# Performance work log

Measured on AMD Instinct MI355X. Metric: run time of the kernel, lower is better.

The kernel has to match this reference:

```python
import jax, jax.numpy as jnp
import numpy as np

N_USER = 50000
N_ITEM = 50000
E = 800000
C_IN = 128
C_OUT = 128
N_HEADS = 4


def setup_inputs() -> dict:
    key = jax.random.key(0)
    ks = jax.random.split(key, 12)
    xav = lambda k, shp: jax.random.uniform(k, shp, jnp.float32, -1.0, 1.0) * jnp.sqrt(6.0 / (shp[0] + shp[1]))
    return {
        'x_user': jax.random.normal(ks[0], (N_USER, C_IN), jnp.float32),
        'x_item': jax.random.normal(ks[1], (N_ITEM, C_IN), jnp.float32),
        'ei_u2i': jnp.stack([jax.random.randint(ks[2], (E,), 0, N_USER, jnp.int32),
                             jax.random.randint(ks[3], (E,), 0, N_ITEM, jnp.int32)]),
        'ei_i2u': jnp.stack([jax.random.randint(ks[4], (E,), 0, N_ITEM, jnp.int32),
                             jax.random.randint(ks[5], (E,), 0, N_USER, jnp.int32)]),
        'W_nb': xav(ks[6], (C_OUT, C_IN)),
        'b_nb': jnp.zeros((C_OUT,), jnp.float32),
        'W_self': xav(ks[7], (C_OUT, C_IN)),
        'b_self': jnp.zeros((C_OUT,), jnp.float32),
        'in_proj_w': xav(ks[8], (3 * C_OUT, C_OUT)),
        'in_proj_b': jnp.zeros((3 * C_OUT,), jnp.float32),
        'out_proj_w': xav(ks[9], (C_OUT, C_OUT)),
        'out_proj_b': jnp.zeros((C_OUT,), jnp.float32),
    }


def _multi_aggr(h_src, edge_index, n_dst):
    """h_src: already lin_neighbor-transformed src features [N_src, C].
    Returns [n_dst, 4, C] stacked as [max, min, sum, mean] (torch_scatter semantics:
    empty segments -> 0; mean divides by clamp(count, 1))."""
    src, dst = edge_index[0], edge_index[1]
    msgs = h_src[src]  # [E, C]  (linear commutes with gather)
    s = jax.ops.segment_sum(msgs, dst, num_segments=n_dst)
    cnt = jax.ops.segment_sum(jnp.ones((msgs.shape[0],), msgs.dtype), dst, num_segments=n_dst)
    has = (cnt > 0)[:, None]
    mean = s / jnp.maximum(cnt, 1.0)[:, None]
    mx = jnp.where(has, jax.ops.segment_max(msgs, dst, num_segments=n_dst), 0.0)
    mn = jnp.where(has, jax.ops.segment_min(msgs, dst, num_segments=n_dst), 0.0)
    return jnp.stack([mx, mn, s, mean], axis=1)  # [n_dst, 4, C]


def _mha(tokens, in_proj_w, in_proj_b, out_proj_w, out_proj_b):
    """torch nn.MultiheadAttention (eval mode, batch_first=False). tokens: [S, N, C]."""
    S, N, C = tokens.shape
    H, Dh = N_HEADS, C // N_HEADS
    qkv = tokens @ in_proj_w.T + in_proj_b            # [S, N, 3C]
    q, k, v = jnp.split(qkv, 3, axis=-1)
    q = q.reshape(S, N, H, Dh) * (1.0 / jnp.sqrt(jnp.asarray(Dh, tokens.dtype)))
    k = k.reshape(S, N, H, Dh)
    v = v.reshape(S, N, H, Dh)
    scores = jnp.einsum('snhd,tnhd->nhst', q, k)       # [N, H, S, S]
    attn = jax.nn.softmax(scores, axis=-1)
    o = jnp.einsum('nhst,tnhd->snhd', attn, v).reshape(S, N, C)
    return o @ out_proj_w.T + out_proj_b               # [S, N, C]


def reference(x_user, x_item, ei_u2i, ei_i2u, W_nb, b_nb, W_self, b_self,
              in_proj_w, in_proj_b, out_proj_w, out_proj_b):
    # shared neighbor linear applied once per node type, then gathered per edge
    h_user = x_user @ W_nb.T + b_nb
    h_item = x_item @ W_nb.T + b_nb
    aggr_item = _multi_aggr(h_user, ei_u2i, N_ITEM)    # user->item : [N_item, 4, C]
    aggr_user = _multi_aggr(h_item, ei_i2u, N_USER)    # item->user : [N_user, 4, C]

    def per_type(x, aggr):
        self_feat = x @ W_self.T + b_self              # [N, C]
        # tokens: [self, max, min, sum, mean] -> [5, N, C]
        tokens = jnp.concatenate([self_feat[None], jnp.transpose(aggr, (1, 0, 2))], axis=0)
        attn_out = _mha(tokens, in_proj_w, in_proj_b, out_proj_w, out_proj_b)
        return self_feat + attn_out.mean(axis=0)

    out_user = per_type(x_user, aggr_user)
    out_item = per_type(x_item, aggr_item)
    return (out_user, out_item)
```

## Files before the change

kernel.cpp:

```cpp
#include <hip/hip_runtime.h>
#include <hip/hip_bf16.h>


#define C 128
#define NHEAD 4
#define DH 32
#define QK_SCALE 0.17677669529663687f

typedef __attribute__((ext_vector_type(8))) short bf16x8;
typedef __attribute__((ext_vector_type(4))) short short4v;
typedef __attribute__((ext_vector_type(2))) short short2v;
typedef __attribute__((ext_vector_type(4))) float f32x4;

__device__ __forceinline__ short f2bf(float f) {
    unsigned u = __float_as_uint(f);
    unsigned r = u + 0x7FFFu + ((u >> 16) & 1u);
    return (short)(r >> 16);
}

__global__ __launch_bounds__(256, 2) void transform_kernel(
    const float* __restrict__ xu, const float* __restrict__ xi,
    int NU, int NTOT,
    const float* __restrict__ Wnb, const float* __restrict__ bnb,
    const float* __restrict__ Wself, const float* __restrict__ bself,
    float* __restrict__ h, float* __restrict__ selfout)
{
    __shared__ float As[64 * 132];
    __shared__ float Bs[256 * 36];
    __shared__ float biasS[256];

    const int tid = threadIdx.x;
    const int row0 = blockIdx.x * 64;

    biasS[tid] = (tid < 128) ? bnb[tid] : bself[tid - 128];

#pragma unroll
    for (int i = 0; i < 8; i++) {
        int id = tid + i * 256;
        int r = id >> 5, c4 = id & 31;
        int row = row0 + r;
        float4 v = make_float4(0.f, 0.f, 0.f, 0.f);
        if (row < NTOT) {
            v = (row < NU) ? ((const float4*)xu)[(size_t)row * 32 + c4]
                           : ((const float4*)xi)[(size_t)(row - NU) * 32 + c4];
        }
        *(float4*)&As[r * 132 + c4 * 4] = v;
    }

    const int tm = tid >> 5;
    const int tn = tid & 31;

    float acc[8][8];
#pragma unroll
    for (int m = 0; m < 8; m++)
#pragma unroll
        for (int j = 0; j < 8; j++) acc[m][j] = 0.f;

    for (int ks = 0; ks < 4; ks++) {
        __syncthreads();
#pragma unroll
        for (int i = 0; i < 8; i++) {
            int id = tid + i * 256;
            int n = id >> 3, q = id & 7;
            const float4* src = (n < 128)
                ? &((const float4*)Wnb)[(size_t)n * 32 + ks * 8 + q]
                : &((const float4*)Wself)[(size_t)(n - 128) * 32 + ks * 8 + q];
            *(float4*)&Bs[n * 36 + q * 4] = *src;
        }
        __syncthreads();

        for (int k4 = 0; k4 < 8; k4++) {
            float4 a[8];
#pragma unroll
            for (int m = 0; m < 8; m++)
                a[m] = *(const float4*)&As[(tm * 8 + m) * 132 + ks * 32 + k4 * 4];
            float4 b[8];
#pragma unroll
            for (int j = 0; j < 8; j++)
                b[j] = *(const float4*)&Bs[(tn + 32 * j) * 36 + k4 * 4];
#pragma unroll
            for (int m = 0; m < 8; m++) {
                float4 av = a[m];
#pragma unroll
                for (int j = 0; j < 8; j++) {
                    float4 bv = b[j];
                    acc[m][j] += av.x * bv.x + av.y * bv.y
                               + av.z * bv.z + av.w * bv.w;
                }
            }
        }
    }

#pragma unroll
    for (int m = 0; m < 8; m++) {
        int row = row0 + tm * 8 + m;
        if (row < NTOT) {
#pragma unroll
            for (int j = 0; j < 8; j++) {
                int jj = tn + 32 * j;
                float v = acc[m][j] + biasS[jj];
                if (j < 4) h[(size_t)row * C + jj] = v;
                else       selfout[(size_t)row * C + (jj - 128)] = v;
            }
        }
    }
}

__global__ __launch_bounds__(256) void prep_kernel(
    const float* __restrict__ Wip, unsigned* __restrict__ img,
    int* __restrict__ curA, int nA, int* __restrict__ curB, int nB)
{
    const int tid = threadIdx.x;
    if (blockIdx.x < 96) {
        int id = blockIdx.x * 256 + tid;
        int ks = id / (384 * 16);
        int rem = id - ks * (384 * 16);
        int n = rem >> 4, kk = rem & 15;
        float a = Wip[(size_t)n * C + ks * 32 + kk * 2 + 0];
        float b = Wip[(size_t)n * C + ks * 32 + kk * 2 + 1];
        unsigned pa = ((unsigned)(unsigned short)f2bf(a))
                    | (((unsigned)(unsigned short)f2bf(b)) << 16);
        img[(size_t)ks * 6144 + n * 16 + kk] = pa;
    } else {
        int i = (blockIdx.x - 96) * 256 + tid;
        if (i < nA) curA[i] = 0;
        else if (i < nA + nB) curB[i - nA] = 0;
    }
}

__global__ __launch_bounds__(256) void hist2_kernel(
    const int* __restrict__ dstA, int nA, int* __restrict__ curA,
    const int* __restrict__ dstB, int nB, int* __restrict__ curB)
{
    int i = blockIdx.x * 256 + threadIdx.x;
    if (i < nA) atomicAdd(&curA[dstA[i]], 1);
    else if (i < nA + nB) atomicAdd(&curB[dstB[i - nA]], 1);
}

__global__ __launch_bounds__(1024) void scan2_kernel(
    int* __restrict__ curA, int nA, int* __restrict__ curB, int nB)
{
    int* cur = (blockIdx.x == 0) ? curA : curB;
    const int n = (blockIdx.x == 0) ? nA : nB;

    __shared__ int wsum[16];
    __shared__ int carryS;
    const int tid = threadIdx.x, lane = tid & 63, wv = tid >> 6;
    if (tid == 0) carryS = 0;
    __syncthreads();
    for (int base = 0; base < n; base += 4096) {
        int i0 = base + tid * 4;
        int v0 = 0, v1 = 0, v2 = 0, v3 = 0;
        if (i0 + 3 < n) {
            int4 t = *(const int4*)&cur[i0];
            v0 = t.x; v1 = t.y; v2 = t.z; v3 = t.w;
        } else {
            if (i0 < n) v0 = cur[i0];
            if (i0 + 1 < n) v1 = cur[i0 + 1];
            if (i0 + 2 < n) v2 = cur[i0 + 2];
            if (i0 + 3 < n) v3 = cur[i0 + 3];
        }
        int s1 = v0 + v1, s2 = s1 + v2, s3 = s2 + v3;
        int x = s3;
#pragma unroll
        for (int d = 1; d < 64; d <<= 1) {
            int t = __shfl_up(x, d, 64);
            if (lane >= d) x += t;
        }
        if (lane == 63) wsum[wv] = x;
        int carry = carryS;
        __syncthreads();
        int wpre = 0;
#pragma unroll
        for (int w2 = 0; w2 < 16; w2++) wpre += (w2 < wv) ? wsum[w2] : 0;
        int excl = x - s3 + wpre + carry;
        if (i0 + 3 < n) {
            int4 st; st.x = excl; st.y = excl + v0; st.z = excl + s1; st.w = excl + s2;
            *(int4*)&cur[i0] = st;
        } else {
            if (i0 < n) cur[i0] = excl;
            if (i0 + 1 < n) cur[i0 + 1] = excl + v0;
            if (i0 + 2 < n) cur[i0 + 2] = excl + s1;
            if (i0 + 3 < n) cur[i0 + 3] = excl + s2;
        }
        __syncthreads();
        if (tid == 0) {
            int t = 0;
#pragma unroll
            for (int w2 = 0; w2 < 16; w2++) t += wsum[w2];
            carryS = carry + t;
        }
        __syncthreads();
    }
}

__global__ __launch_bounds__(256) void fill_kernel(
    const int* __restrict__ src, const int* __restrict__ dst, int n,
    int* __restrict__ cur, int* __restrict__ csr)
{
    int i = blockIdx.x * 256 + threadIdx.x;
    if (i < n) {
        int p = atomicAdd(&cur[dst[i]], 1);
        csr[p] = src[i];
    }
}

#define ATN 4

__global__ __launch_bounds__(256, 8) void attn_fused_kernel(
    const float* __restrict__ h_src, const int* __restrict__ csr,
    const int* __restrict__ cur, const float* __restrict__ selfF,
    const short* __restrict__ wipbf, const float* __restrict__ bip,
    float* __restrict__ omean_g, int n_nodes)
{
    __shared__ char Ash[16 * 272];
    __shared__ float cinv[ATN];

    const int tid = threadIdx.x;
    const int lane = tid & 63;
    const int wv = tid >> 6;
    const int node0 = blockIdx.x * ATN;

    if (tid < 128) {
        int r = tid >> 5, c4 = tid & 31;
        int node = node0 + r;
        float4 v = make_float4(0.f, 0.f, 0.f, 0.f);
        if (node < n_nodes) v = ((const float4*)selfF)[(size_t)node * 32 + c4];
        short4v b;
        b.x = f2bf(v.x); b.y = f2bf(v.y); b.z = f2bf(v.z); b.w = f2bf(v.w);
        *(short4v*)(Ash + (r * 4) * 272 + c4 * 8) = b;
    }

    {
        const float2* h2 = (const float2*)h_src;
        int node = node0 + wv;
        float2 vs = make_float2(0.f, 0.f);
        float2 vmx = make_float2(-3.4e38f, -3.4e38f);
        float2 vmn = make_float2(3.4e38f, 3.4e38f);
        int deg = 0;
        if (node < n_nodes) {
            int start = (node == 0) ? 0 : cur[node - 1];
            int end = cur[node];
            deg = end - start;
            int e = start;
            for (; e + 8 <= end; e += 8) {
                float2 v[8];
#pragma unroll
                for (int i = 0; i < 8; i++) {
                    int s = csr[e + i];
                    v[i] = h2[(size_t)s * 64 + lane];
                }
#pragma unroll
                for (int i = 0; i < 8; i++) {
                    vs.x += v[i].x; vs.y += v[i].y;
                    vmx.x = fmaxf(vmx.x, v[i].x); vmx.y = fmaxf(vmx.y, v[i].y);
                    vmn.x = fminf(vmn.x, v[i].x); vmn.y = fminf(vmn.y, v[i].y);
                }
            }
            if (e < end) {
                int last = end - 1;
                float2 v[8];
#pragma unroll
                for (int i = 0; i < 8; i++) {
                    int idx = e + i;
                    int s = csr[(idx <= last) ? idx : last];
                    v[i] = h2[(size_t)s * 64 + lane];
                }
#pragma unroll
                for (int i = 0; i < 8; i++) {
                    if (e + i <= last) {
                        vs.x += v[i].x; vs.y += v[i].y;
                        vmx.x = fmaxf(vmx.x, v[i].x); vmx.y = fmaxf(vmx.y, v[i].y);
                        vmn.x = fminf(vmn.x, v[i].x); vmn.y = fminf(vmn.y, v[i].y);
                    }
                }
            }
        }
        if (deg == 0) {
            vmx = make_float2(0.f, 0.f);
            vmn = make_float2(0.f, 0.f);
        }
        short2v p;
        p.x = f2bf(vmx.x); p.y = f2bf(vmx.y);
        *(short2v*)(Ash + (wv * 4 + 1) * 272 + lane * 4) = p;
        p.x = f2bf(vmn.x); p.y = f2bf(vmn.y);
        *(short2v*)(Ash + (wv * 4 + 2) * 272 + lane * 4) = p;
        p.x = f2bf(vs.x); p.y = f2bf(vs.y);
        *(short2v*)(Ash + (wv * 4 + 3) * 272 + lane * 4) = p;
        if (lane == 0) cinv[wv] = 1.f / (float)max(deg, 1);
    }
    __syncthreads();

    const int quad = lane >> 4;
    const int col16 = lane & 15;

    f32x4 acc[6];
#pragma unroll
    for (int t = 0; t < 6; t++) acc[t] = (f32x4){0.f, 0.f, 0.f, 0.f};

#pragma unroll
    for (int ks = 0; ks < 4; ks++) {
        bf16x8 af = *(const bf16x8*)(Ash + col16 * 272 + ks * 64 + quad * 16);
#pragma unroll
        for (int t = 0; t < 6; t++) {
            int nb = wv * 32 + (t & 1) * 16 + (t >> 1) * 128 + col16;
            bf16x8 bfr = *(const bf16x8*)((const char*)wipbf
                          + (size_t)ks * 24576 + (size_t)nb * 64 + quad * 16);
            acc[t] = __builtin_amdgcn_mfma_f32_16x16x32_bf16(af, bfr, acc[t], 0, 0, 0);
        }
    }

    const float ci = cinv[quad];
    const float cis = ci * QK_SCALE;

    const float bq0 = bip[wv * 32 + col16];
    const float bq1 = bip[wv * 32 + 16 + col16];
    const float bk0 = bip[128 + wv * 32 + col16];
    const float bk1 = bip[128 + wv * 32 + 16 + col16];
    const float bv0 = bip[256 + wv * 32 + col16];
    const float bv1 = bip[256 + wv * 32 + 16 + col16];
    const float bq0s = bq0 * QK_SCALE;
    const float bq1s = bq1 * QK_SCALE;

    float k0[5], k1[5];
#pragma unroll
    for (int s = 0; s < 4; s++) { k0[s] = acc[2][s] + bk0; k1[s] = acc[3][s] + bk1; }
    k0[4] = fmaf(acc[2][3], ci, bk0);
    k1[4] = fmaf(acc[3][3], ci, bk1);

    float wj[5] = {0.f, 0.f, 0.f, 0.f, 0.f};
#pragma unroll
    for (int i = 0; i < 5; i++) {
        float qi0 = (i < 4) ? fmaf(acc[0][i], QK_SCALE, bq0s)
                            : fmaf(acc[0][3], cis, bq0s);
        float qi1 = (i < 4) ? fmaf(acc[1][i], QK_SCALE, bq1s)
                            : fmaf(acc[1][3], cis, bq1s);
        float sv[5];
#pragma unroll
        for (int j = 0; j < 5; j++) sv[j] = qi0 * k0[j] + qi1 * k1[j];
#pragma unroll
        for (int j = 0; j < 5; j++) {
            sv[j] += __shfl_xor(sv[j], 1, 16);
            sv[j] += __shfl_xor(sv[j], 2, 16);
            sv[j] += __shfl_xor(sv[j], 4, 16);
            sv[j] += __shfl_xor(sv[j], 8, 16);
        }
        float m = sv[0];
#pragma unroll
        for (int j = 1; j < 5; j++) m = fmaxf(m, sv[j]);
        float e[5], l = 0.f;
#pragma unroll
        for (int j = 0; j < 5; j++) { e[j] = __expf(sv[j] - m); l += e[j]; }
        float inv = 0.2f / l;
#pragma unroll
        for (int j = 0; j < 5; j++) wj[j] = fmaf(e[j], inv, wj[j]);
    }

    float o0 = 0.f, o1 = 0.f;
#pragma unroll
    for (int j = 0; j < 5; j++) {
        float v0 = (j < 4) ? (acc[4][j] + bv0) : fmaf(acc[4][3], ci, bv0);
        float v1 = (j < 4) ? (acc[5][j] + bv1) : fmaf(acc[5][3], ci, bv1);
        o0 = fmaf(wj[j], v0, o0);
        o1 = fmaf(wj[j], v1, o1);
    }

    int node = node0 + quad;
    if (node < n_nodes) {
        omean_g[(size_t)node * C + wv * 32 + col16] = o0;
        omean_g[(size_t)node * C + wv * 32 + 16 + col16] = o1;
    }
}

__global__ __launch_bounds__(256, 3) void outproj_kernel(
    const float* __restrict__ omean_g, const float* __restrict__ Wop,
    const float* __restrict__ bop, float* __restrict__ out, int M)
{
    __shared__ float As[64 * 132];
    __shared__ float Bs[128 * 36];
    __shared__ float bopS[C];

    const int tid = threadIdx.x;
    const int m0 = blockIdx.x * 64;

    if (tid < C) bopS[tid] = bop[tid];

#pragma unroll
    for (int i = 0; i < 8; i++) {
        int id = tid + i * 256;
        int r = id >> 5, c4 = id & 31;
        float4 v = make_float4(0.f, 0.f, 0.f, 0.f);
        if (m0 + r < M) v = ((const float4*)omean_g)[(size_t)(m0 + r) * 32 + c4];
        *(float4*)&As[r * 132 + c4 * 4] = v;
    }

    const int tm = tid >> 5;
    const int tn = tid & 31;

    float acc[8][4];
#pragma unroll
    for (int m = 0; m < 8; m++)
#pragma unroll
        for (int j = 0; j < 4; j++) acc[m][j] = 0.f;

    for (int ks = 0; ks < 4; ks++) {
        __syncthreads();
#pragma unroll
        for (int i = 0; i < 4; i++) {
            int id = tid + i * 256;
            int n = id >> 3, q = id & 7;
            float4 w = ((const float4*)Wop)[(size_t)n * 32 + ks * 8 + q];
            *(float4*)&Bs[n * 36 + q * 4] = w;
        }
        __syncthreads();

        for (int k4 = 0; k4 < 8; k4++) {
            float4 a[8];
#pragma unroll
            for (int m = 0; m < 8; m++)
                a[m] = *(const float4*)&As[(tm * 8 + m) * 132 + ks * 32 + k4 * 4];
            float4 b[4];
#pragma unroll
            for (int j = 0; j < 4; j++)
                b[j] = *(const float4*)&Bs[(tn + 32 * j) * 36 + k4 * 4];
#pragma unroll
            for (int m = 0; m < 8; m++) {
                float4 av = a[m];
#pragma unroll
                for (int j = 0; j < 4; j++) {
                    float4 bv = b[j];
                    acc[m][j] += av.x * bv.x + av.y * bv.y
                               + av.z * bv.z + av.w * bv.w;
                }
            }
        }
    }

#pragma unroll
    for (int m = 0; m < 8; m++) {
        int row = m0 + tm * 8 + m;
        if (row < M) {
#pragma unroll
            for (int j = 0; j < 4; j++) {
                int col = tn + 32 * j;
                float* o = &out[(size_t)row * C + col];
                *o += acc[m][j] + bopS[col];
            }
        }
    }
}

extern "C" void kernel_launch(void* const* d_in, const int* in_sizes, int n_in,
                              void* d_out, int out_size, void* d_ws, size_t ws_size,
                              hipStream_t stream) {
    const float* x_user = (const float*)d_in[0];
    const float* x_item = (const float*)d_in[1];
    const int*   ei_u2i = (const int*)d_in[2];
    const int*   ei_i2u = (const int*)d_in[3];
    const float* W_nb   = (const float*)d_in[4];
    const float* b_nb   = (const float*)d_in[5];
    const float* W_self = (const float*)d_in[6];
    const float* b_self = (const float*)d_in[7];
    const float* Wip    = (const float*)d_in[8];
    const float* bip    = (const float*)d_in[9];
    const float* Wop    = (const float*)d_in[10];
    const float* bop    = (const float*)d_in[11];

    const int NU = in_sizes[0] / C;
    const int NI = in_sizes[1] / C;
    const int E1 = in_sizes[2] / 2;
    const int E2 = in_sizes[3] / 2;
    const int NTOT = NU + NI;

    float* out_user = (float*)d_out;
    float* out_item = out_user + (size_t)NU * C;

    float* ws = (float*)d_ws;
    short* wipbf     = (short*)ws;
    float* h_all     = ws + 24576;
    const size_t rc = (size_t)NTOT * C;
    float* omean_all = h_all + rc;
    int*   curA      = (int*)(omean_all + rc);
    const int maxN   = (NU > NI) ? NU : NI;
    int*   csr       = curA + maxN;

    float* h_user = h_all;
    float* h_item = h_all + (size_t)NU * C;
    float* om_user = omean_all;
    float* om_item = omean_all + (size_t)NU * C;
    int*   curB    = (int*)om_item;

    prep_kernel<<<96 + (NTOT + 255) / 256, 256, 0, stream>>>(
        Wip, (unsigned*)wipbf, curA, NI, curB, NU);

    transform_kernel<<<(NTOT + 63) / 64, 256, 0, stream>>>(
        x_user, x_item, NU, NTOT, W_nb, b_nb, W_self, b_self, h_all, (float*)d_out);

    hist2_kernel<<<(E1 + E2 + 255) / 256, 256, 0, stream>>>(
        ei_u2i + E1, E1, curA, ei_i2u + E2, E2, curB);

    scan2_kernel<<<2, 1024, 0, stream>>>(curA, NI, curB, NU);

    fill_kernel<<<(E2 + 255) / 256, 256, 0, stream>>>(ei_i2u, ei_i2u + E2, E2, curB, csr);
    attn_fused_kernel<<<(NU + ATN - 1) / ATN, 256, 0, stream>>>(
        h_item, csr, curB, out_user, wipbf, bip, om_user, NU);

    fill_kernel<<<(E1 + 255) / 256, 256, 0, stream>>>(ei_u2i, ei_u2i + E1, E1, curA, csr);
    attn_fused_kernel<<<(NI + ATN - 1) / ATN, 256, 0, stream>>>(
        h_user, csr, curA, out_item, wipbf, bip, om_item, NI);

    outproj_kernel<<<(NTOT + 63) / 64, 256, 0, stream>>>(
        omean_all, Wop, bop, (float*)d_out, NTOT);
}
```

Measured before the change: 696.3 us.

## Merge launches, use 16-bit CSR indices, process 8 nodes per attention block

Folds the weight-prep and counter-zeroing kernel into the transform kernel as extra blocks. It also merges both fill kernels and both attention kernels into single launches over the two edge directions. CSR source indices are stored as 16-bit values to cut index traffic, and each attention block now handles 8 nodes, with each wave aggregating two nodes and running two MFMA row tiles. The aim is fewer launches and better overlap between directions. The cost is more register pressure, lower occupancy, and reliance on node counts fitting in 16 bits: 50000 does fit, but larger graphs would break.

```diff
diff --git a/kernel.cpp b/kernel.cpp
--- a/kernel.cpp
+++ b/kernel.cpp
@@ -18,18 +18,41 @@
     return (short)(r >> 16);
 }
 
-__global__ __launch_bounds__(256, 2) void transform_kernel(
+__global__ __launch_bounds__(256, 2) void transform_prep_kernel(
     const float* __restrict__ xu, const float* __restrict__ xi,
     int NU, int NTOT,
     const float* __restrict__ Wnb, const float* __restrict__ bnb,
     const float* __restrict__ Wself, const float* __restrict__ bself,
-    float* __restrict__ h, float* __restrict__ selfout)
+    float* __restrict__ h, float* __restrict__ selfout,
+    const float* __restrict__ Wip, unsigned* __restrict__ img,
+    int* __restrict__ curA, int nA, int* __restrict__ curB, int nB, int TB)
 {
+    const int tid = threadIdx.x;
+
+    if ((int)blockIdx.x >= TB) {
+        int bid2 = (int)blockIdx.x - TB;
+        if (bid2 < 96) {
+            int id = bid2 * 256 + tid;
+            int ks = id / (384 * 16);
+            int rem = id - ks * (384 * 16);
+            int n = rem >> 4, kk = rem & 15;
+            float a = Wip[(size_t)n * C + ks * 32 + kk * 2 + 0];
+            float b = Wip[(size_t)n * C + ks * 32 + kk * 2 + 1];
+            unsigned pa = ((unsigned)(unsigned short)f2bf(a))
+                        | (((unsigned)(unsigned short)f2bf(b)) << 16);
+            img[(size_t)ks * 6144 + n * 16 + kk] = pa;
+        } else {
+            int i = (bid2 - 96) * 256 + tid;
+            if (i < nA) curA[i] = 0;
+            else if (i < nA + nB) curB[i - nA] = 0;
+        }
+        return;
+    }
+
     __shared__ float As[64 * 132];
     __shared__ float Bs[256 * 36];
     __shared__ float biasS[256];
 
-    const int tid = threadIdx.x;
     const int row0 = blockIdx.x * 64;
 
     biasS[tid] = (tid < 128) ? bnb[tid] : bself[tid - 128];
@@ -103,28 +126,6 @@
                 else       selfout[(size_t)row * C + (jj - 128)] = v;
             }
         }
-    }
-}
-
-__global__ __launch_bounds__(256) void prep_kernel(
-    const float* __restrict__ Wip, unsigned* __restrict__ img,
-    int* __restrict__ curA, int nA, int* __restrict__ curB, int nB)
-{
-    const int tid = threadIdx.x;
-    if (blockIdx.x < 96) {
-        int id = blockIdx.x * 256 + tid;
-        int ks = id / (384 * 16);
-        int rem = id - ks * (384 * 16);
-        int n = rem >> 4, kk = rem & 15;
-        float a = Wip[(size_t)n * C + ks * 32 + kk * 2 + 0];
-        float b = Wip[(size_t)n * C + ks * 32 + kk * 2 + 1];
-        unsigned pa = ((unsigned)(unsigned short)f2bf(a))
-                    | (((unsigned)(unsigned short)f2bf(b)) << 16);
-        img[(size_t)ks * 6144 + n * 16 + kk] = pa;
-    } else {
-        int i = (blockIdx.x - 96) * 256 + tid;
-        if (i < nA) curA[i] = 0;
-        else if (i < nA + nB) curB[i - nA] = 0;
     }
 }
 
@@ -194,34 +195,52 @@
     }
 }
 
-__global__ __launch_bounds__(256) void fill_kernel(
-    const int* __restrict__ src, const int* __restrict__ dst, int n,
-    int* __restrict__ cur, int* __restrict__ csr)
+__global__ __launch_bounds__(256) void fill2_kernel(
+    const int* __restrict__ srcA, const int* __restrict__ dstA, int nA,
+    int* __restrict__ curA, unsigned short* __restrict__ csrA,
+    const int* __restrict__ srcB, const int* __restrict__ dstB, int nB,
+    int* __restrict__ curB, unsigned short* __restrict__ csrB)
 {
     int i = blockIdx.x * 256 + threadIdx.x;
-    if (i < n) {
-        int p = atomicAdd(&cur[dst[i]], 1);
-        csr[p] = src[i];
-    }
-}
-
-#define ATN 4
-
-__global__ __launch_bounds__(256, 8) void attn_fused_kernel(
-    const float* __restrict__ h_src, const int* __restrict__ csr,
-    const int* __restrict__ cur, const float* __restrict__ selfF,
-    const short* __restrict__ wipbf, const float* __restrict__ bip,
-    float* __restrict__ omean_g, int n_nodes)
+    if (i < nA) {
+        int p = atomicAdd(&curA[dstA[i]], 1);
+        csrA[p] = (unsigned short)srcA[i];
+    } else if (i < nA + nB) {
+        int j = i - nA;
+        int p = atomicAdd(&curB[dstB[j]], 1);
+        csrB[p] = (unsigned short)srcB[j];
+    }
+}
+
+#define ATN 8
+
+__global__ __launch_bounds__(256, 6) void attn2_kernel(
+    const float* __restrict__ hB, const unsigned short* __restrict__ csrB,
+    const int* __restrict__ curB, const float* __restrict__ selfB,
+    float* __restrict__ omB, int nNodesB, int nbB,
+    const float* __restrict__ hA, const unsigned short* __restrict__ csrA,
+    const int* __restrict__ curA, const float* __restrict__ selfA,
+    float* __restrict__ omA, int nNodesA,
+    const short* __restrict__ wipbf, const float* __restrict__ bip)
 {
-    __shared__ char Ash[16 * 272];
+    __shared__ char Ash[32 * 272];
     __shared__ float cinv[ATN];
 
     const int tid = threadIdx.x;
     const int lane = tid & 63;
     const int wv = tid >> 6;
-    const int node0 = blockIdx.x * ATN;
-
-    if (tid < 128) {
+
+    const int bid = (int)blockIdx.x;
+    const bool dirB = bid < nbB;
+    const float* h_src = dirB ? hB : hA;
+    const unsigned short* csr = dirB ? csrB : csrA;
+    const int* cur = dirB ? curB : curA;
+    const float* selfF = dirB ? selfB : selfA;
+    float* omean_g = dirB ? omB : omA;
+    const int n_nodes = dirB ? nNodesB : nNodesA;
+    const int node0 = (dirB ? bid : bid - nbB) * ATN;
+
+    {
         int r = tid >> 5, c4 = tid & 31;
         int node = node0 + r;
         float4 v = make_float4(0.f, 0.f, 0.f, 0.f);
@@ -231,9 +250,11 @@
         *(short4v*)(Ash + (r * 4) * 272 + c4 * 8) = b;
     }
 
-    {
-        const float2* h2 = (const float2*)h_src;
-        int node = node0 + wv;
+    const float2* h2 = (const float2*)h_src;
+#pragma unroll
+    for (int half = 0; half < 2; half++) {
+        int nl = wv * 2 + half;
+        int node = node0 + nl;
         float2 vs = make_float2(0.f, 0.f);
         float2 vmx = make_float2(-3.4e38f, -3.4e38f);
         float2 vmn = make_float2(3.4e38f, 3.4e38f);
@@ -282,36 +303,37 @@
         }
         short2v p;
         p.x = f2bf(vmx.x); p.y = f2bf(vmx.y);
-        *(short2v*)(Ash + (wv * 4 + 1) * 272 + lane * 4) = p;
+        *(short2v*)(Ash + (nl * 4 + 1) * 272 + lane * 4) = p;
         p.x = f2bf(vmn.x); p.y = f2bf(vmn.y);
-        *(short2v*)(Ash + (wv * 4 + 2) * 272 + lane * 4) = p;
+        *(short2v*)(Ash + (nl * 4 + 2) * 272 + lane * 4) = p;
         p.x = f2bf(vs.x); p.y = f2bf(vs.y);
-        *(short2v*)(Ash + (wv * 4 + 3) * 272 + lane * 4) = p;
-        if (lane == 0) cinv[wv] = 1.f / (float)max(deg, 1);
+        *(short2v*)(Ash + (nl * 4 + 3) * 272 + lane * 4) = p;
+        if (lane == 0) cinv[nl] = 1.f / (float)max(deg, 1);
     }
     __syncthreads();
 
     const int quad = lane >> 4;
     const int col16 = lane & 15;
 
-    f32x4 acc[6];
-#pragma unroll
-    for (int t = 0; t < 6; t++) acc[t] = (f32x4){0.f, 0.f, 0.f, 0.f};
+    f32x4 acc[2][6];
+#pragma unroll
+    for (int m = 0; m < 2; m++)
+#pragma unroll
+        for (int t = 0; t < 6; t++) acc[m][t] = (f32x4){0.f, 0.f, 0.f, 0.f};
 
 #pragma unroll
     for (int ks = 0; ks < 4; ks++) {
-        bf16x8 af = *(const bf16x8*)(Ash + col16 * 272 + ks * 64 + quad * 16);
+        bf16x8 af0 = *(const bf16x8*)(Ash + col16 * 272 + ks * 64 + quad * 16);
+        bf16x8 af1 = *(const bf16x8*)(Ash + (16 + col16) * 272 + ks * 64 + quad * 16);
 #pragma unroll
         for (int t = 0; t < 6; t++) {
             int nb = wv * 32 + (t & 1) * 16 + (t >> 1) * 128 + col16;
             bf16x8 bfr = *(const bf16x8*)((const char*)wipbf
                           + (size_t)ks * 24576 + (size_t)nb * 64 + quad * 16);
-            acc[t] = __builtin_amdgcn_mfma_f32_16x16x32_bf16(af, bfr, acc[t], 0, 0, 0);
-        }
-    }
-
-    const float ci = cinv[quad];
-    const float cis = ci * QK_SCALE;
+            acc[0][t] = __builtin_amdgcn_mfma_f32_16x16x32_bf16(af0, bfr, acc[0][t], 0, 0, 0);
+            acc[1][t] = __builtin_amdgcn_mfma_f32_16x16x32_bf16(af1, bfr, acc[1][t], 0, 0, 0);
+        }
+    }
 
     const float bq0 = bip[wv * 32 + col16];
     const float bq1 = bip[wv * 32 + 16 + col16];
@@ -322,53 +344,62 @@
     const float bq0s = bq0 * QK_SCALE;
     const float bq1s = bq1 * QK_SCALE;
 
-    float k0[5], k1[5];
-#pragma unroll
-    for (int s = 0; s < 4; s++) { k0[s] = acc[2][s] + bk0; k1[s] = acc[3][s] + bk1; }
-    k0[4] = fmaf(acc[2][3], ci, bk0);
-    k1[4] = fmaf(acc[3][3], ci, bk1);
-
-    float wj[5] = {0.f, 0.f, 0.f, 0.f, 0.f};
-#pragma unroll
-    for (int i = 0; i < 5; i++) {
-        float qi0 = (i < 4) ? fmaf(acc[0][i], QK_SCALE, bq0s)
-                            : fmaf(acc[0][3], cis, bq0s);
-        float qi1 = (i < 4) ? fmaf(acc[1][i], QK_SCALE, bq1s)
-                            : fmaf(acc[1][3], cis, bq1s);
-        float sv[5];
-#pragma unroll
-        for (int j = 0; j < 5; j++) sv[j] = qi0 * k0[j] + qi1 * k1[j];
+#pragma unroll
+    for (int m = 0; m < 2; m++) {
+        const float ci = cinv[m * 4 + quad];
+        const float cis = ci * QK_SCALE;
+
+        float k0[5], k1[5];
+#pragma unroll
+        for (int s = 0; s < 4; s++) {
+            k0[s] = acc[m][2][s] + bk0;
+            k1[s] = acc[m][3][s] + bk1;
+        }
+        k0[4] = fmaf(acc[m][2][3], ci, bk0);
+        k1[4] = fmaf(acc[m][3][3], ci, bk1);
+
+        float wj[5] = {0.f, 0.f, 0.f, 0.f, 0.f};
+#pragma unroll
+        for (int i = 0; i < 5; i++) {
+            float qi0 = (i < 4) ? fmaf(acc[m][0][i], QK_SCALE, bq0s)
+                                : fmaf(acc[m][0][3], cis, bq0s);
+            float qi1 = (i < 4) ? fmaf(acc[m][1][i], QK_SCALE, bq1s)
+                                : fmaf(acc[m][1][3], cis, bq1s);
+            float sv[5];
+#pragma unroll
+            for (int j = 0; j < 5; j++) sv[j] = qi0 * k0[j] + qi1 * k1[j];
+#pragma unroll
+            for (int j = 0; j < 5; j++) {
+                sv[j] += __shfl_xor(sv[j], 1, 16);
+                sv[j] += __shfl_xor(sv[j], 2, 16);
+                sv[j] += __shfl_xor(sv[j], 4, 16);
+                sv[j] += __shfl_xor(sv[j], 8, 16);
+            }
+            float mx = sv[0];
+#pragma unroll
+            for (int j = 1; j < 5; j++) mx = fmaxf(mx, sv[j]);
+            float e[5], l = 0.f;
+#pragma unroll
+            for (int j = 0; j < 5; j++) { e[j] = __expf(sv[j] - mx); l += e[j]; }
+            float inv = 0.2f / l;
+#pragma unroll
+            for (int j = 0; j < 5; j++) wj[j] = fmaf(e[j], inv, wj[j]);
+        }
+
+        float o0 = 0.f, o1 = 0.f;
 #pragma unroll
         for (int j = 0; j < 5; j++) {
-            sv[j] += __shfl_xor(sv[j], 1, 16);
-            sv[j] += __shfl_xor(sv[j], 2, 16);
-            sv[j] += __shfl_xor(sv[j], 4, 16);
-            sv[j] += __shfl_xor(sv[j], 8, 16);
-        }
-        float m = sv[0];
-#pragma unroll
-        for (int j = 1; j < 5; j++) m = fmaxf(m, sv[j]);
-        float e[5], l = 0.f;
-#pragma unroll
-        for (int j = 0; j < 5; j++) { e[j] = __expf(sv[j] - m); l += e[j]; }
-        float inv = 0.2f / l;
-#pragma unroll
-        for (int j = 0; j < 5; j++) wj[j] = fmaf(e[j], inv, wj[j]);
-    }
-
-    float o0 = 0.f, o1 = 0.f;
-#pragma unroll
-    for (int j = 0; j < 5; j++) {
-        float v0 = (j < 4) ? (acc[4][j] + bv0) : fmaf(acc[4][3], ci, bv0);
-        float v1 = (j < 4) ? (acc[5][j] + bv1) : fmaf(acc[5][3], ci, bv1);
-        o0 = fmaf(wj[j], v0, o0);
-        o1 = fmaf(wj[j], v1, o1);
-    }
-
-    int node = node0 + quad;
-    if (node < n_nodes) {
-        omean_g[(size_t)node * C + wv * 32 + col16] = o0;
-        omean_g[(size_t)node * C + wv * 32 + 16 + col16] = o1;
+            float v0 = (j < 4) ? (acc[m][4][j] + bv0) : fmaf(acc[m][4][3], ci, bv0);
+            float v1 = (j < 4) ? (acc[m][5][j] + bv1) : fmaf(acc[m][5][3], ci, bv1);
+            o0 = fmaf(wj[j], v0, o0);
+            o1 = fmaf(wj[j], v1, o1);
+        }
+
+        int node = node0 + m * 4 + quad;
+        if (node < n_nodes) {
+            omean_g[(size_t)node * C + wv * 32 + col16] = o0;
+            omean_g[(size_t)node * C + wv * 32 + 16 + col16] = o1;
+        }
     }
 }
 
@@ -394,9 +425,8 @@
         *(float4*)&As[r * 132 + c4 * 4] = v;
     }
 
+    const int tn = tid & 31;
     const int tm = tid >> 5;
-    const int tn = tid & 31;
-
     float acc[8][4];
 #pragma unroll
     for (int m = 0; m < 8; m++)
@@ -481,33 +511,36 @@
     const size_t rc = (size_t)NTOT * C;
     float* omean_all = h_all + rc;
     int*   curA      = (int*)(omean_all + rc);
-    const int maxN   = (NU > NI) ? NU : NI;
-    int*   csr       = curA + maxN;
+    int*   curB      = curA + NI;
+    unsigned short* csrA16 = (unsigned short*)(curB + NU);
+    unsigned short* csrB16 = csrA16 + E1;
 
     float* h_user = h_all;
     float* h_item = h_all + (size_t)NU * C;
     float* om_user = omean_all;
     float* om_item = omean_all + (size_t)NU * C;
-    int*   curB    = (int*)om_item;
-
-    prep_kernel<<<96 + (NTOT + 255) / 256, 256, 0, stream>>>(
-        Wip, (unsigned*)wipbf, curA, NI, curB, NU);
-
-    transform_kernel<<<(NTOT + 63) / 64, 256, 0, stream>>>(
-        x_user, x_item, NU, NTOT, W_nb, b_nb, W_self, b_self, h_all, (float*)d_out);
+
+    const int TB = (NTOT + 63) / 64;
+    const int PB = 96 + (NTOT + 255) / 256;
+    transform_prep_kernel<<<TB + PB, 256, 0, stream>>>(
+        x_user, x_item, NU, NTOT, W_nb, b_nb, W_self, b_self,
+        h_all, (float*)d_out, Wip, (unsigned*)wipbf, curA, NI, curB, NU, TB);
 
     hist2_kernel<<<(E1 + E2 + 255) / 256, 256, 0, stream>>>(
         ei_u2i + E1, E1, curA, ei_i2u + E2, E2, curB);
 
     scan2_kernel<<<2, 1024, 0, stream>>>(curA, NI, curB, NU);
 
-    fill_kernel<<<(E2 + 255) / 256, 256, 0, stream>>>(ei_i2u, ei_i2u + E2, E2, curB, csr);
-    attn_fused_kernel<<<(NU + ATN - 1) / ATN, 256, 0, stream>>>(
-        h_item, csr, curB, out_user, wipbf, bip, om_user, NU);
-
-    fill_kernel<<<(E1 + 255) / 256, 256, 0, stream>>>(ei_u2i, ei_u2i + E1, E1, curA, csr);
-    attn_fused_kernel<<<(NI + ATN - 1) / ATN, 256, 0, stream>>>(
-        h_user, csr, curA, out_item, wipbf, bip, om_item, NI);
+    fill2_kernel<<<(E1 + E2 + 255) / 256, 256, 0, stream>>>(
+        ei_u2i, ei_u2i + E1, E1, curA, csrA16,
+        ei_i2u, ei_i2u + E2, E2, curB, csrB16);
+
+    const int nbB = (NU + ATN - 1) / ATN;
+    const int nbA = (NI + ATN - 1) / ATN;
+    attn2_kernel<<<nbB + nbA, 256, 0, stream>>>(
+        h_item, csrB16, curB, out_user, om_user, NU, nbB,
+        h_user, csrA16, curA, out_item, om_item, NI,
+        wipbf, bip);
 
     outproj_kernel<<<(NTOT + 63) / 64, 256, 0, stream>>>(
         omean_all, Wop, bop, (float*)d_out, NTOT);
```

Measured after the change: 788.7 us. 13.3% more time.

## Fuse prep into transform, merge CSR fills, store CSR indices as uint16

Applied to the files above, without the earlier changes.

Folds the weight bf16 packing and counter zeroing into extra blocks of the transform kernel, and builds both CSR arrays in one fill kernel, removing two launches. Each edge type now gets its own CSR buffer, and source indices are stored as 16-bit values. This halves index traffic in the gather-heavy attention kernels. The uint16 indices only work while node counts stay at or below 65535, which holds for the fixed problem sizes.

```diff
diff --git a/kernel.cpp b/kernel.cpp
--- a/kernel.cpp
+++ b/kernel.cpp
@@ -18,18 +18,41 @@
     return (short)(r >> 16);
 }
 
-__global__ __launch_bounds__(256, 2) void transform_kernel(
+__global__ __launch_bounds__(256, 2) void transform_prep_kernel(
     const float* __restrict__ xu, const float* __restrict__ xi,
     int NU, int NTOT,
     const float* __restrict__ Wnb, const float* __restrict__ bnb,
     const float* __restrict__ Wself, const float* __restrict__ bself,
-    float* __restrict__ h, float* __restrict__ selfout)
+    float* __restrict__ h, float* __restrict__ selfout,
+    const float* __restrict__ Wip, unsigned* __restrict__ img,
+    int* __restrict__ curA, int nA, int* __restrict__ curB, int nB, int TB)
 {
+    const int tid = threadIdx.x;
+
+    if ((int)blockIdx.x >= TB) {
+        int bid2 = (int)blockIdx.x - TB;
+        if (bid2 < 96) {
+            int id = bid2 * 256 + tid;
+            int ks = id / (384 * 16);
+            int rem = id - ks * (384 * 16);
+            int n = rem >> 4, kk = rem & 15;
+            float a = Wip[(size_t)n * C + ks * 32 + kk * 2 + 0];
+            float b = Wip[(size_t)n * C + ks * 32 + kk * 2 + 1];
+            unsigned pa = ((unsigned)(unsigned short)f2bf(a))
+                        | (((unsigned)(unsigned short)f2bf(b)) << 16);
+            img[(size_t)ks * 6144 + n * 16 + kk] = pa;
+        } else {
+            int i = (bid2 - 96) * 256 + tid;
+            if (i < nA) curA[i] = 0;
+            else if (i < nA + nB) curB[i - nA] = 0;
+        }
+        return;
+    }
+
     __shared__ float As[64 * 132];
     __shared__ float Bs[256 * 36];
     __shared__ float biasS[256];
 
-    const int tid = threadIdx.x;
     const int row0 = blockIdx.x * 64;
 
     biasS[tid] = (tid < 128) ? bnb[tid] : bself[tid - 128];
@@ -103,28 +126,6 @@
                 else       selfout[(size_t)row * C + (jj - 128)] = v;
             }
         }
-    }
-}
-
-__global__ __launch_bounds__(256) void prep_kernel(
-    const float* __restrict__ Wip, unsigned* __restrict__ img,
-    int* __restrict__ curA, int nA, int* __restrict__ curB, int nB)
-{
-    const int tid = threadIdx.x;
-    if (blockIdx.x < 96) {
-        int id = blockIdx.x * 256 + tid;
-        int ks = id / (384 * 16);
-        int rem = id - ks * (384 * 16);
-        int n = rem >> 4, kk = rem & 15;
-        float a = Wip[(size_t)n * C + ks * 32 + kk * 2 + 0];
-        float b = Wip[(size_t)n * C + ks * 32 + kk * 2 + 1];
-        unsigned pa = ((unsigned)(unsigned short)f2bf(a))
-                    | (((unsigned)(unsigned short)f2bf(b)) << 16);
-        img[(size_t)ks * 6144 + n * 16 + kk] = pa;
-    } else {
-        int i = (blockIdx.x - 96) * 256 + tid;
-        if (i < nA) curA[i] = 0;
-        else if (i < nA + nB) curB[i - nA] = 0;
     }
 }
 
@@ -194,21 +195,27 @@
     }
 }
 
-__global__ __launch_bounds__(256) void fill_kernel(
-    const int* __restrict__ src, const int* __restrict__ dst, int n,
-    int* __restrict__ cur, int* __restrict__ csr)
+__global__ __launch_bounds__(256) void fill2_kernel(
+    const int* __restrict__ srcA, const int* __restrict__ dstA, int nA,
+    int* __restrict__ curA, unsigned short* __restrict__ csrA,
+    const int* __restrict__ srcB, const int* __restrict__ dstB, int nB,
+    int* __restrict__ curB, unsigned short* __restrict__ csrB)
 {
     int i = blockIdx.x * 256 + threadIdx.x;
-    if (i < n) {
-        int p = atomicAdd(&cur[dst[i]], 1);
-        csr[p] = src[i];
+    if (i < nA) {
+        int p = atomicAdd(&curA[dstA[i]], 1);
+        csrA[p] = (unsigned short)srcA[i];
+    } else if (i < nA + nB) {
+        int j = i - nA;
+        int p = atomicAdd(&curB[dstB[j]], 1);
+        csrB[p] = (unsigned short)srcB[j];
     }
 }
 
 #define ATN 4
 
 __global__ __launch_bounds__(256, 8) void attn_fused_kernel(
-    const float* __restrict__ h_src, const int* __restrict__ csr,
+    const float* __restrict__ h_src, const unsigned short* __restrict__ csr,
     const int* __restrict__ cur, const float* __restrict__ selfF,
     const short* __restrict__ wipbf, const float* __restrict__ bip,
     float* __restrict__ omean_g, int n_nodes)
@@ -394,9 +401,8 @@
         *(float4*)&As[r * 132 + c4 * 4] = v;
     }
 
+    const int tn = tid & 31;
     const int tm = tid >> 5;
-    const int tn = tid & 31;
-
     float acc[8][4];
 #pragma unroll
     for (int m = 0; m < 8; m++)
@@ -481,33 +487,35 @@
     const size_t rc = (size_t)NTOT * C;
     float* omean_all = h_all + rc;
     int*   curA      = (int*)(omean_all + rc);
-    const int maxN   = (NU > NI) ? NU : NI;
-    int*   csr       = curA + maxN;
+    int*   curB      = curA + NI;
+    unsigned short* csrA16 = (unsigned short*)(curB + NU);
+    unsigned short* csrB16 = csrA16 + E1;
 
     float* h_user = h_all;
     float* h_item = h_all + (size_t)NU * C;
     float* om_user = omean_all;
     float* om_item = omean_all + (size_t)NU * C;
-    int*   curB    = (int*)om_item;
-
-    prep_kernel<<<96 + (NTOT + 255) / 256, 256, 0, stream>>>(
-        Wip, (unsigned*)wipbf, curA, NI, curB, NU);
-
-    transform_kernel<<<(NTOT + 63) / 64, 256, 0, stream>>>(
-        x_user, x_item, NU, NTOT, W_nb, b_nb, W_self, b_self, h_all, (float*)d_out);
+
+    const int TB = (NTOT + 63) / 64;
+    const int PB = 96 + (NTOT + 255) / 256;
+    transform_prep_kernel<<<TB + PB, 256, 0, stream>>>(
+        x_user, x_item, NU, NTOT, W_nb, b_nb, W_self, b_self,
+        h_all, (float*)d_out, Wip, (unsigned*)wipbf, curA, NI, curB, NU, TB);
 
     hist2_kernel<<<(E1 + E2 + 255) / 256, 256, 0, stream>>>(
         ei_u2i + E1, E1, curA, ei_i2u + E2, E2, curB);
 
     scan2_kernel<<<2, 1024, 0, stream>>>(curA, NI, curB, NU);
 
-    fill_kernel<<<(E2 + 255) / 256, 256, 0, stream>>>(ei_i2u, ei_i2u + E2, E2, curB, csr);
+    fill2_kernel<<<(E1 + E2 + 255) / 256, 256, 0, stream>>>(
+        ei_u2i, ei_u2i + E1, E1, curA, csrA16,
+        ei_i2u, ei_i2u + E2, E2, curB, csrB16);
+
     attn_fused_kernel<<<(NU + ATN - 1) / ATN, 256, 0, stream>>>(
-        h_item, csr, curB, out_user, wipbf, bip, om_user, NU);
-
-    fill_kernel<<<(E1 + 255) / 256, 256, 0, stream>>>(ei_u2i, ei_u2i + E1, E1, curA, csr);
+        h_item, csrB16, curB, out_user, wipbf, bip, om_user, NU);
+
     attn_fused_kernel<<<(NI + ATN - 1) / ATN, 256, 0, stream>>>(
-        h_user, csr, curA, out_item, wipbf, bip, om_item, NI);
+        h_user, csrA16, curA, out_item, wipbf, bip, om_item, NI);
 
     outproj_kernel<<<(NTOT + 63) / 64, 256, 0, stream>>>(
         omean_all, Wop, bop, (float*)d_out, NTOT);
```

Result: no change. 706.8 us (+1.5%).
